# Kernel optimization log

Hardware: AMD Instinct MI355X
Metric: run time of the kernel (lower is better)

The kernel has to match this reference:

```python
import jax, jax.numpy as jnp
import numpy as np

SCALE = 768.0  # scale = output_features


def setup_inputs() -> dict:
    key = jax.random.key(0)
    k1, k2, k3, k4 = jax.random.split(key, 4)
    B, S, D, F = 8, 2048, 768, 768
    x = jax.random.normal(k1, (B, S, D), dtype=jnp.float32)
    # torch nn.Linear weights: shape (out_features, in_features), y = x @ W.T
    Wq = jax.random.normal(k2, (F, D), dtype=jnp.float32) * (1.0 / np.sqrt(D))
    Wk = jax.random.normal(k3, (F, D), dtype=jnp.float32) * (1.0 / np.sqrt(D))
    Wv = jax.random.normal(k4, (F, D), dtype=jnp.float32) * (1.0 / np.sqrt(D))
    return {"x": x, "Wq": Wq, "Wk": Wk, "Wv": Wv}


def _cdist_l2(q, k):
    # pairwise Euclidean distances, [B, S, S]; matches torch.cdist(q, k, p=2)
    q2 = jnp.sum(q * q, axis=-1)  # [B, S]
    k2 = jnp.sum(k * k, axis=-1)  # [B, S]
    qk = jnp.einsum('bid,bjd->bij', q, k)  # [B, S, S]
    d2 = q2[:, :, None] + k2[:, None, :] - 2.0 * qk
    return jnp.sqrt(jnp.maximum(d2, 0.0))


def reference(x, Wq, Wk, Wv):
    q = jnp.einsum('bsd,fd->bsf', x, Wq)
    k = jnp.einsum('bsd,fd->bsf', x, Wk)
    v = jnp.einsum('bsd,fd->bsf', x, Wv)
    scores = _cdist_l2(q, k) / jnp.sqrt(jnp.asarray(SCALE, dtype=x.dtype))
    attn = jax.nn.softmax(scores, axis=-1)  # NOTE: source softmaxes raw distances (no negation)
    return jnp.einsum('bij,bjf->bif', attn, v)
```

## Files before the change

kernel.cpp:

```cpp
#include <hip/hip_runtime.h>
#include <stdint.h>
#include <math.h>


typedef __attribute__((ext_vector_type(8))) __bf16 bf16x8;
typedef __attribute__((ext_vector_type(4))) float f32x4;
typedef __attribute__((ext_vector_type(4))) unsigned int u32x4;

__device__ __forceinline__ unsigned short f2b(float f) {
    unsigned u = __float_as_uint(f);
    unsigned r = 0x7fffu + ((u >> 16) & 1u);
    return (unsigned short)((u + r) >> 16);
}
__device__ __forceinline__ float b2f(unsigned short h) {
    return __uint_as_float(((unsigned)h) << 16);
}

__device__ __forceinline__ void wg_barrier() {
    asm volatile("" ::: "memory");
    __builtin_amdgcn_s_barrier();
    asm volatile("" ::: "memory");
}

__device__ __forceinline__ unsigned lds_off(const void* p) {
    return (unsigned)(uintptr_t)(const __attribute__((address_space(3))) char*)p;
}

__global__ __launch_bounds__(256) void castk(const float* __restrict__ src,
                                             unsigned short* __restrict__ dst, int n4) {
    int i = blockIdx.x * 256 + threadIdx.x;
    if (i >= n4) return;
    float4 v = ((const float4*)src)[i];
    ushort4 o;
    o.x = f2b(v.x); o.y = f2b(v.y); o.z = f2b(v.z); o.w = f2b(v.w);
    ((ushort4*)dst)[i] = o;
}

template <int MODE>
__global__ __launch_bounds__(256) void rowreduce(const unsigned short* __restrict__ X,
                                                 int L, int rows, float* __restrict__ out) {
    int w = threadIdx.x >> 6, lane = threadIdx.x & 63;
    int row = blockIdx.x * 4 + w;
    if (row >= rows) return;
    const unsigned short* xr = X + (size_t)row * L;
    float s = 0.f;
    int passes = L >> 8;
    for (int p = 0; p < passes; ++p) {
        ushort4 u = *(const ushort4*)(xr + (p << 8) + lane * 4);
        float a = b2f(u.x), b = b2f(u.y), c = b2f(u.z), d = b2f(u.w);
        s += MODE ? (a * a + b * b + c * c + d * d) : (a + b + c + d);
    }
#pragma unroll
    for (int o = 32; o > 0; o >>= 1) s += __shfl_down(s, o);
    if (lane == 0) out[row] = s;
}

#define MF(A_, B_, C_) (C_) = __builtin_amdgcn_mfma_f32_16x16x32_bf16((A_), (B_), (C_), 0, 0, 0)
#define DSR(dst_, a_, imm_) \
    asm volatile("ds_read_b128 %0, %1 offset:" #imm_ : "=v"(dst_) : "v"(a_))
#define GL4(d_, p_) asm volatile("global_load_dwordx4 %0, %1, off" : "=v"(d_) : "v"(p_))
#define DSW(a_, imm_, d_) \
    asm volatile("ds_write_b128 %0, %1 offset:" #imm_ :: "v"(a_), "v"(d_) : "memory")
#define LGKM(n_) asm volatile("s_waitcnt lgkmcnt(" #n_ ")" ::: "memory")
#define VMC0 asm volatile("s_waitcnt vmcnt(0)" ::: "memory")
#define SB0 __builtin_amdgcn_sched_barrier(0)

#define LOADT(T_) do {                                                     \
    const size_t ko_ = (size_t)(T_) * 64;                                  \
    GL4(ra0, pa + ko_);             GL4(ra1, pa + lda64 + ko_);            \
    GL4(ra2, pa + 2 * lda64 + ko_); GL4(ra3, pa + 3 * lda64 + ko_);        \
    GL4(rb0, pb + ko_);             GL4(rb1, pb + ldb64 + ko_);            \
    GL4(rb2, pb + 2 * ldb64 + ko_); GL4(rb3, pb + 3 * ldb64 + ko_);        \
} while (0)
#define WRITET(WB_) do {                                                   \
    const unsigned wa_ = wA + (WB_), wb2_ = wB + (WB_);                    \
    DSW(wa_, 0, ra0);     DSW(wa_, 8192, ra1);                             \
    DSW(wa_, 16384, ra2); DSW(wa_, 24576, ra3);                            \
    DSW(wb2_, 0, rb0);     DSW(wb2_, 8192, rb1);                           \
    DSW(wb2_, 16384, rb2); DSW(wb2_, 24576, rb3);                          \
} while (0)

template <int EPI>
__global__ __launch_bounds__(512, 2) void gemm256(
    const unsigned short* __restrict__ A, int lda, long long sA,
    const unsigned short* __restrict__ B, int ldb, long long sB,
    void* __restrict__ Cv, int ldc, long long sC,
    int Kd, int perm,
    const float* __restrict__ aux1, int sAux1,
    const float* __restrict__ aux2, int sAux2,
    float invs) {
    __shared__ __attribute__((aligned(128))) unsigned short As[2 * 256 * 64];
    __shared__ __attribute__((aligned(128))) unsigned short Bs[2 * 256 * 64];

    const int z = perm ? blockIdx.x : blockIdx.z;
    const int jb = perm ? blockIdx.y : blockIdx.x;
    const int ib = perm ? blockIdx.z : blockIdx.y;
    const unsigned short* __restrict__ Ab = A + (size_t)z * sA;
    const unsigned short* __restrict__ Bb = B + (size_t)z * sB;
    const int i0 = ib * 256;
    const int j0 = jb * 256;
    const int tid = threadIdx.x;
    const int w = tid >> 6, lane = tid & 63;
    const int wr = w >> 2, wc = w & 3;
    const int c16 = lane & 15, kq = lane >> 4;

    const int lr0 = tid >> 3;
    const int clog0 = (tid & 7) ^ (lr0 & 7);
    const unsigned short* pa = Ab + (size_t)(i0 + lr0) * lda + clog0 * 8;
    const unsigned short* pb = Bb + (size_t)(j0 + lr0) * ldb + clog0 * 8;
    const size_t lda64 = (size_t)64 * lda, ldb64 = (size_t)64 * ldb;

    const unsigned wA = lds_off(As) + (unsigned)tid * 16;
    const unsigned wB = lds_off(Bs) + (unsigned)tid * 16;

    const int swc = (kq ^ (c16 & 7)) << 4;
    const unsigned adrA0 = lds_off(As) + (unsigned)(wr * 128 + c16) * 128 + swc;
    const unsigned adrA0x = adrA0 ^ 64u;
    const unsigned adrB0 = lds_off(Bs) + (unsigned)(wc * 64 + c16) * 128 + swc;
    const unsigned adrB0x = adrB0 ^ 64u;

    f32x4 acc[8][4];
    const f32x4 zero = {0.f, 0.f, 0.f, 0.f};
#pragma unroll
    for (int i = 0; i < 8; ++i)
#pragma unroll
        for (int j = 0; j < 4; ++j) acc[i][j] = zero;

    u32x4 ra0, ra1, ra2, ra3, rb0, rb1, rb2, rb3;
    bf16x8 aL[4][2], aH[4][2], bF[4][2];

    const int nt = Kd >> 6;

    LOADT(0);
    VMC0;
    WRITET(0u);
    LOADT(1);
    LGKM(0);
    wg_barrier();

    for (int t = 0; t < nt; ++t) {
        const unsigned rb_ = (t & 1) ? 32768u : 0u;
        const unsigned wb_ = (t & 1) ? 0u : 32768u;
        const unsigned aA = adrA0 + rb_, aAx = adrA0x + rb_;
        const unsigned aB = adrB0 + rb_, aBx = adrB0x + rb_;
        DSR(aL[0][0], aA, 0);    DSR(aL[0][1], aAx, 0);
        DSR(aL[1][0], aA, 2048); DSR(aL[1][1], aAx, 2048);
        DSR(aL[2][0], aA, 4096); DSR(aL[2][1], aAx, 4096);
        DSR(aL[3][0], aA, 6144); DSR(aL[3][1], aAx, 6144);
        DSR(bF[0][0], aB, 0);    DSR(bF[0][1], aBx, 0);
        DSR(bF[1][0], aB, 2048); DSR(bF[1][1], aBx, 2048);
        DSR(bF[2][0], aB, 4096); DSR(bF[2][1], aBx, 4096);
        DSR(bF[3][0], aB, 6144); DSR(bF[3][1], aBx, 6144);
        if (t + 1 < nt) {
            VMC0;
            WRITET(wb_);
            if (t + 2 < nt) LOADT(t + 2);
            LGKM(8);
        } else {
            LGKM(0);
        }
        SB0;
        __builtin_amdgcn_s_setprio(1);
#pragma unroll
        for (int kk = 0; kk < 2; ++kk)
#pragma unroll
            for (int mi = 0; mi < 4; ++mi)
#pragma unroll
                for (int ni = 0; ni < 4; ++ni)
                    MF(aL[mi][kk], bF[ni][kk], acc[mi][ni]);
        __builtin_amdgcn_s_setprio(0);
        DSR(aH[0][0], aA, 8192);  DSR(aH[0][1], aAx, 8192);
        DSR(aH[1][0], aA, 10240); DSR(aH[1][1], aAx, 10240);
        DSR(aH[2][0], aA, 12288); DSR(aH[2][1], aAx, 12288);
        DSR(aH[3][0], aA, 14336); DSR(aH[3][1], aAx, 14336);
        LGKM(0); SB0;
        __builtin_amdgcn_s_setprio(1);
#pragma unroll
        for (int kk = 0; kk < 2; ++kk)
#pragma unroll
            for (int mi = 0; mi < 4; ++mi)
#pragma unroll
                for (int ni = 0; ni < 4; ++ni)
                    MF(aH[mi][kk], bF[ni][kk], acc[4 + mi][ni]);
        __builtin_amdgcn_s_setprio(0);
        wg_barrier();
    }

    const int r4 = kq * 4;
    if constexpr (EPI == 0) {
        unsigned short* C = (unsigned short*)Cv + (size_t)z * sC;
#pragma unroll
        for (int mi = 0; mi < 8; ++mi)
#pragma unroll
            for (int ni = 0; ni < 4; ++ni) {
                const int row = i0 + wr * 128 + mi * 16 + r4;
                const int col = j0 + wc * 64 + ni * 16 + c16;
#pragma unroll
                for (int r = 0; r < 4; ++r)
                    C[(size_t)(row + r) * ldc + col] = f2b(acc[mi][ni][r]);
            }
    } else if constexpr (EPI == 1) {
        unsigned short* C = (unsigned short*)Cv + (size_t)z * sC;
        const float* q2b = aux1 + (size_t)z * sAux1;
        const float* k2b = aux2 + (size_t)z * sAux2;
#pragma unroll
        for (int mi = 0; mi < 8; ++mi)
#pragma unroll
            for (int ni = 0; ni < 4; ++ni) {
                const int row = i0 + wr * 128 + mi * 16 + r4;
                const int col = j0 + wc * 64 + ni * 16 + c16;
                const float k2v = k2b[col];
#pragma unroll
                for (int r = 0; r < 4; ++r) {
                    float d2 = q2b[row + r] + k2v - 2.0f * acc[mi][ni][r];
                    float e = __expf(sqrtf(fmaxf(d2, 0.f)) * invs);
                    C[(size_t)(row + r) * ldc + col] = f2b(e);
                }
            }
    } else {
        float* C = (float*)Cv + (size_t)z * sC;
        const float* lb = aux1 + (size_t)z * sAux1;
#pragma unroll
        for (int mi = 0; mi < 8; ++mi)
#pragma unroll
            for (int ni = 0; ni < 4; ++ni) {
                const int row = i0 + wr * 128 + mi * 16 + r4;
                const int col = j0 + wc * 64 + ni * 16 + c16;
#pragma unroll
                for (int r = 0; r < 4; ++r)
                    C[(size_t)(row + r) * ldc + col] = acc[mi][ni][r] / lb[row + r];
            }
    }
}

extern "C" void kernel_launch(void* const* d_in, const int* in_sizes, int n_in,
                              void* d_out, int out_size, void* d_ws, size_t ws_size,
                              hipStream_t stream) {
    const float* x = (const float*)d_in[0];
    const float* Wq = (const float*)d_in[1];
    const float* Wk = (const float*)d_in[2];
    const float* Wv = (const float*)d_in[3];
    const int Bz = 8, S = 2048, D = 768, F = 768;
    const int BS = Bz * S;

    const size_t szX = (size_t)BS * D * 2;
    const size_t szW = (size_t)F * D * 2;
    const size_t szE = (size_t)Bz * S * S * 2;

    char* p = (char*)d_ws;
    unsigned short* xb = (unsigned short*)p;  p += szX;
    unsigned short* Wqb = (unsigned short*)p; p += szW;
    unsigned short* Wkb = (unsigned short*)p; p += szW;
    unsigned short* Wvb = (unsigned short*)p; p += szW;
    unsigned short* Qm = (unsigned short*)p;  p += szX;
    unsigned short* Km = (unsigned short*)p;  p += szX;
    unsigned short* VT = (unsigned short*)p;  p += szX;
    unsigned short* E = (unsigned short*)p;   p += szE;
    float* q2 = (float*)p;   p += (size_t)BS * 4;
    float* k2 = (float*)p;   p += (size_t)BS * 4;
    float* lsum = (float*)p; p += (size_t)BS * 4;
    if ((size_t)(p - (char*)d_ws) > ws_size) return;

    const float invs = 1.0f / sqrtf(768.0f);

    castk<<<(BS * D / 4 + 255) / 256, 256, 0, stream>>>(x, xb, BS * D / 4);
    castk<<<(F * D / 4 + 255) / 256, 256, 0, stream>>>(Wq, Wqb, F * D / 4);
    castk<<<(F * D / 4 + 255) / 256, 256, 0, stream>>>(Wk, Wkb, F * D / 4);
    castk<<<(F * D / 4 + 255) / 256, 256, 0, stream>>>(Wv, Wvb, F * D / 4);

    gemm256<0><<<dim3(F / 256, BS / 256, 2), 512, 0, stream>>>(
        xb, D, 0,
        Wqb, D, (long long)F * D,
        Qm, F, (long long)BS * F,
        D, 0, nullptr, 0, nullptr, 0, 0.f);

    gemm256<0><<<dim3(BS / 256, F / 256, 1), 512, 0, stream>>>(
        Wvb, D, 0,
        xb, D, 0,
        VT, BS, 0,
        D, 0, nullptr, 0, nullptr, 0, 0.f);

    rowreduce<1><<<BS / 4, 256, 0, stream>>>(Qm, F, BS, q2);
    rowreduce<1><<<BS / 4, 256, 0, stream>>>(Km, F, BS, k2);

    gemm256<1><<<dim3(Bz, S / 256, S / 256), 512, 0, stream>>>(
        Qm, F, (long long)S * F,
        Km, F, (long long)S * F,
        E, S, (long long)S * S,
        F, 1, q2, S, k2, S, invs);

    rowreduce<0><<<BS / 4, 256, 0, stream>>>(E, S, BS, lsum);

    gemm256<2><<<dim3(Bz, F / 256, S / 256), 512, 0, stream>>>(
        E, S, (long long)S * S,
        VT, BS, (long long)S,
        d_out, F, (long long)S * F,
        S, 1, lsum, S, nullptr, 0, 0.f);
}
```

Measured before the change: 254.1 us.

## Store Q and K in FP8 and compute distance GEMM with FP8 MFMA

The Q/K projection now writes FP8 e4m3 outputs instead of bf16. A new FP8 GEMM kernel computes QK^T using fp8 MFMA with half-width LDS tiles and loads, and fuses the exp(dist) epilogue. Row norms are computed from the FP8 values so they stay consistent with the dot products. This halves Q/K memory traffic and uses the higher-throughput FP8 matrix path, at the cost of precision. Distance errors feed straight into the exponent, so correctness tolerance is at risk.

```diff
diff --git a/kernel.cpp b/kernel.cpp
--- a/kernel.cpp
+++ b/kernel.cpp
@@ -1,4 +1,5 @@
 #include <hip/hip_runtime.h>
+#include <hip/hip_fp8.h>
 #include <stdint.h>
 #include <math.h>
 
@@ -6,6 +7,7 @@
 typedef __attribute__((ext_vector_type(8))) __bf16 bf16x8;
 typedef __attribute__((ext_vector_type(4))) float f32x4;
 typedef __attribute__((ext_vector_type(4))) unsigned int u32x4;
+typedef __attribute__((ext_vector_type(2))) unsigned int u32x2;
 
 __device__ __forceinline__ unsigned short f2b(float f) {
     unsigned u = __float_as_uint(f);
@@ -14,6 +16,15 @@
 }
 __device__ __forceinline__ float b2f(unsigned short h) {
     return __uint_as_float(((unsigned)h) << 16);
+}
+__device__ __forceinline__ unsigned char f2f8(float f) {
+    __hip_fp8_e4m3 t(f);
+    return t.__x;
+}
+__device__ __forceinline__ float f8tof(unsigned char b) {
+    int e = (b >> 3) & 15, m = b & 7;
+    float v = e ? ldexpf(8.0f + m, e - 10) : ldexpf((float)m, -9);
+    return (b & 0x80) ? -v : v;
 }
 
 __device__ __forceinline__ void wg_barrier() {
@@ -55,12 +66,36 @@
     if (lane == 0) out[row] = s;
 }
 
+__global__ __launch_bounds__(256) void rowreduce8(const unsigned char* __restrict__ X,
+                                                  int L, int rows, float* __restrict__ out) {
+    int w = threadIdx.x >> 6, lane = threadIdx.x & 63;
+    int row = blockIdx.x * 4 + w;
+    if (row >= rows) return;
+    const unsigned char* xr = X + (size_t)row * L;
+    float s = 0.f;
+    int passes = L >> 8;
+    for (int p = 0; p < passes; ++p) {
+        uchar4 u = *(const uchar4*)(xr + (p << 8) + lane * 4);
+        float a = f8tof(u.x), b = f8tof(u.y), c = f8tof(u.z), d = f8tof(u.w);
+        s += a * a + b * b + c * c + d * d;
+    }
+#pragma unroll
+    for (int o = 32; o > 0; o >>= 1) s += __shfl_down(s, o);
+    if (lane == 0) out[row] = s;
+}
+
 #define MF(A_, B_, C_) (C_) = __builtin_amdgcn_mfma_f32_16x16x32_bf16((A_), (B_), (C_), 0, 0, 0)
+#define MF8(A_, B_, C_) (C_) = __builtin_amdgcn_mfma_f32_16x16x32_fp8_fp8((A_), (B_), (C_), 0, 0, 0)
 #define DSR(dst_, a_, imm_) \
     asm volatile("ds_read_b128 %0, %1 offset:" #imm_ : "=v"(dst_) : "v"(a_))
+#define DSR64(dst_, a_, imm_) \
+    asm volatile("ds_read_b64 %0, %1 offset:" #imm_ : "=v"(dst_) : "v"(a_))
 #define GL4(d_, p_) asm volatile("global_load_dwordx4 %0, %1, off" : "=v"(d_) : "v"(p_))
+#define GL2(d_, p_) asm volatile("global_load_dwordx2 %0, %1, off" : "=v"(d_) : "v"(p_))
 #define DSW(a_, imm_, d_) \
     asm volatile("ds_write_b128 %0, %1 offset:" #imm_ :: "v"(a_), "v"(d_) : "memory")
+#define DSW64(a_, imm_, d_) \
+    asm volatile("ds_write_b64 %0, %1 offset:" #imm_ :: "v"(a_), "v"(d_) : "memory")
 #define LGKM(n_) asm volatile("s_waitcnt lgkmcnt(" #n_ ")" ::: "memory")
 #define VMC0 asm volatile("s_waitcnt vmcnt(0)" ::: "memory")
 #define SB0 __builtin_amdgcn_sched_barrier(0)
@@ -86,9 +121,7 @@
     const unsigned short* __restrict__ B, int ldb, long long sB,
     void* __restrict__ Cv, int ldc, long long sC,
     int Kd, int perm,
-    const float* __restrict__ aux1, int sAux1,
-    const float* __restrict__ aux2, int sAux2,
-    float invs) {
+    const float* __restrict__ aux1, int sAux1) {
     __shared__ __attribute__((aligned(128))) unsigned short As[2 * 256 * 64];
     __shared__ __attribute__((aligned(128))) unsigned short Bs[2 * 256 * 64];
 
@@ -97,8 +130,7 @@
     const int ib = perm ? blockIdx.z : blockIdx.y;
     const unsigned short* __restrict__ Ab = A + (size_t)z * sA;
     const unsigned short* __restrict__ Bb = B + (size_t)z * sB;
-    const int i0 = ib * 256;
-    const int j0 = jb * 256;
+    const int i0 = ib * 256, j0 = jb * 256;
     const int tid = threadIdx.x;
     const int w = tid >> 6, lane = tid & 63;
     const int wr = w >> 2, wc = w & 3;
@@ -199,23 +231,17 @@
                 for (int r = 0; r < 4; ++r)
                     C[(size_t)(row + r) * ldc + col] = f2b(acc[mi][ni][r]);
             }
-    } else if constexpr (EPI == 1) {
-        unsigned short* C = (unsigned short*)Cv + (size_t)z * sC;
-        const float* q2b = aux1 + (size_t)z * sAux1;
-        const float* k2b = aux2 + (size_t)z * sAux2;
+    } else if constexpr (EPI == 3) {
+        unsigned char* C = (unsigned char*)Cv + (size_t)z * sC;
 #pragma unroll
         for (int mi = 0; mi < 8; ++mi)
 #pragma unroll
             for (int ni = 0; ni < 4; ++ni) {
                 const int row = i0 + wr * 128 + mi * 16 + r4;
                 const int col = j0 + wc * 64 + ni * 16 + c16;
-                const float k2v = k2b[col];
-#pragma unroll
-                for (int r = 0; r < 4; ++r) {
-                    float d2 = q2b[row + r] + k2v - 2.0f * acc[mi][ni][r];
-                    float e = __expf(sqrtf(fmaxf(d2, 0.f)) * invs);
-                    C[(size_t)(row + r) * ldc + col] = f2b(e);
-                }
+#pragma unroll
+                for (int r = 0; r < 4; ++r)
+                    C[(size_t)(row + r) * ldc + col] = f2f8(acc[mi][ni][r]);
             }
     } else {
         float* C = (float*)Cv + (size_t)z * sC;
@@ -231,6 +257,144 @@
                     C[(size_t)(row + r) * ldc + col] = acc[mi][ni][r] / lb[row + r];
             }
     }
+}
+
+#define LOADT8(T_) do {                                                    \
+    const size_t ko_ = (size_t)(T_) * 64;                                  \
+    GL2(fa0, pa8 + ko_);              GL2(fa1, pa8 + lda64b + ko_);        \
+    GL2(fa2, pa8 + 2 * lda64b + ko_); GL2(fa3, pa8 + 3 * lda64b + ko_);    \
+    GL2(fb0, pb8 + ko_);              GL2(fb1, pb8 + ldb64b + ko_);        \
+    GL2(fb2, pb8 + 2 * ldb64b + ko_); GL2(fb3, pb8 + 3 * ldb64b + ko_);    \
+} while (0)
+#define WRITET8(WB_) do {                                                  \
+    const unsigned wa_ = wA8 + (WB_), wb2_ = wB8 + (WB_);                  \
+    DSW64(wa_, 0, fa0);     DSW64(wa_, 4096, fa1);                         \
+    DSW64(wa_, 8192, fa2);  DSW64(wa_, 12288, fa3);                        \
+    DSW64(wb2_, 0, fb0);    DSW64(wb2_, 4096, fb1);                        \
+    DSW64(wb2_, 8192, fb2); DSW64(wb2_, 12288, fb3);                       \
+} while (0)
+
+__global__ __launch_bounds__(512, 2) void gemm256f8(
+    const unsigned char* __restrict__ A, int lda, long long sA,
+    const unsigned char* __restrict__ B, int ldb, long long sB,
+    unsigned short* __restrict__ Cq, int ldc, long long sC,
+    int Kd,
+    const float* __restrict__ q2a, int sQ2,
+    const float* __restrict__ k2a, int sK2,
+    float invs) {
+    __shared__ __attribute__((aligned(128))) unsigned char As8[2 * 256 * 64];
+    __shared__ __attribute__((aligned(128))) unsigned char Bs8[2 * 256 * 64];
+
+    const int z = blockIdx.x;
+    const int jb = blockIdx.y, ib = blockIdx.z;
+    const unsigned char* __restrict__ Ab = A + (size_t)z * sA;
+    const unsigned char* __restrict__ Bb = B + (size_t)z * sB;
+    const int i0 = ib * 256, j0 = jb * 256;
+    const int tid = threadIdx.x;
+    const int w = tid >> 6, lane = tid & 63;
+    const int wr = w >> 2, wc = w & 3;
+    const int c16 = lane & 15, kq = lane >> 4;
+
+    const int lr0 = tid >> 3;
+    const int slog = (tid & 7) ^ (lr0 & 7);
+    const unsigned char* pa8 = Ab + (size_t)(i0 + lr0) * lda + slog * 8;
+    const unsigned char* pb8 = Bb + (size_t)(j0 + lr0) * ldb + slog * 8;
+    const size_t lda64b = (size_t)64 * lda, ldb64b = (size_t)64 * ldb;
+
+    const unsigned wA8 = lds_off(As8) + (unsigned)tid * 8;
+    const unsigned wB8 = lds_off(Bs8) + (unsigned)tid * 8;
+
+    const int sw8 = (kq ^ (c16 & 7)) << 3;
+    const unsigned adrA0 = lds_off(As8) + (unsigned)(wr * 128 + c16) * 64 + sw8;
+    const unsigned adrA0x = adrA0 ^ 32u;
+    const unsigned adrB0 = lds_off(Bs8) + (unsigned)(wc * 64 + c16) * 64 + sw8;
+    const unsigned adrB0x = adrB0 ^ 32u;
+
+    f32x4 acc[8][4];
+    const f32x4 zero = {0.f, 0.f, 0.f, 0.f};
+#pragma unroll
+    for (int i = 0; i < 8; ++i)
+#pragma unroll
+        for (int j = 0; j < 4; ++j) acc[i][j] = zero;
+
+    u32x2 fa0, fa1, fa2, fa3, fb0, fb1, fb2, fb3;
+    long aL[4][2], aH[4][2], bF[4][2];
+
+    const int nt = Kd >> 6;
+
+    LOADT8(0);
+    VMC0;
+    WRITET8(0u);
+    LOADT8(1);
+    LGKM(0);
+    wg_barrier();
+
+    for (int t = 0; t < nt; ++t) {
+        const unsigned rb_ = (t & 1) ? 16384u : 0u;
+        const unsigned wb_ = (t & 1) ? 0u : 16384u;
+        const unsigned aA = adrA0 + rb_, aAx = adrA0x + rb_;
+        const unsigned aB = adrB0 + rb_, aBx = adrB0x + rb_;
+        DSR64(aL[0][0], aA, 0);    DSR64(aL[0][1], aAx, 0);
+        DSR64(aL[1][0], aA, 1024); DSR64(aL[1][1], aAx, 1024);
+        DSR64(aL[2][0], aA, 2048); DSR64(aL[2][1], aAx, 2048);
+        DSR64(aL[3][0], aA, 3072); DSR64(aL[3][1], aAx, 3072);
+        DSR64(bF[0][0], aB, 0);    DSR64(bF[0][1], aBx, 0);
+        DSR64(bF[1][0], aB, 1024); DSR64(bF[1][1], aBx, 1024);
+        DSR64(bF[2][0], aB, 2048); DSR64(bF[2][1], aBx, 2048);
+        DSR64(bF[3][0], aB, 3072); DSR64(bF[3][1], aBx, 3072);
+        if (t + 1 < nt) {
+            VMC0;
+            WRITET8(wb_);
+            if (t + 2 < nt) LOADT8(t + 2);
+            LGKM(8);
+        } else {
+            LGKM(0);
+        }
+        SB0;
+        __builtin_amdgcn_s_setprio(1);
+#pragma unroll
+        for (int kk = 0; kk < 2; ++kk)
+#pragma unroll
+            for (int mi = 0; mi < 4; ++mi)
+#pragma unroll
+                for (int ni = 0; ni < 4; ++ni)
+                    MF8(aL[mi][kk], bF[ni][kk], acc[mi][ni]);
+        __builtin_amdgcn_s_setprio(0);
+        DSR64(aH[0][0], aA, 4096); DSR64(aH[0][1], aAx, 4096);
+        DSR64(aH[1][0], aA, 5120); DSR64(aH[1][1], aAx, 5120);
+        DSR64(aH[2][0], aA, 6144); DSR64(aH[2][1], aAx, 6144);
+        DSR64(aH[3][0], aA, 7168); DSR64(aH[3][1], aAx, 7168);
+        LGKM(0); SB0;
+        __builtin_amdgcn_s_setprio(1);
+#pragma unroll
+        for (int kk = 0; kk < 2; ++kk)
+#pragma unroll
+            for (int mi = 0; mi < 4; ++mi)
+#pragma unroll
+                for (int ni = 0; ni < 4; ++ni)
+                    MF8(aH[mi][kk], bF[ni][kk], acc[4 + mi][ni]);
+        __builtin_amdgcn_s_setprio(0);
+        wg_barrier();
+    }
+
+    const int r4 = kq * 4;
+    unsigned short* C = Cq + (size_t)z * sC;
+    const float* q2b = q2a + (size_t)z * sQ2;
+    const float* k2b = k2a + (size_t)z * sK2;
+#pragma unroll
+    for (int mi = 0; mi < 8; ++mi)
+#pragma unroll
+        for (int ni = 0; ni < 4; ++ni) {
+            const int row = i0 + wr * 128 + mi * 16 + r4;
+            const int col = j0 + wc * 64 + ni * 16 + c16;
+            const float k2v = k2b[col];
+#pragma unroll
+            for (int r = 0; r < 4; ++r) {
+                float d2 = q2b[row + r] + k2v - 2.0f * acc[mi][ni][r];
+                float e = __expf(sqrtf(fmaxf(d2, 0.f)) * invs);
+                C[(size_t)(row + r) * ldc + col] = f2b(e);
+            }
+        }
 }
 
 extern "C" void kernel_launch(void* const* d_in, const int* in_sizes, int n_in,
@@ -245,6 +409,7 @@
 
     const size_t szX = (size_t)BS * D * 2;
     const size_t szW = (size_t)F * D * 2;
+    const size_t szQ8 = (size_t)BS * F;
     const size_t szE = (size_t)Bz * S * S * 2;
 
     char* p = (char*)d_ws;
@@ -252,8 +417,8 @@
     unsigned short* Wqb = (unsigned short*)p; p += szW;
     unsigned short* Wkb = (unsigned short*)p; p += szW;
     unsigned short* Wvb = (unsigned short*)p; p += szW;
-    unsigned short* Qm = (unsigned short*)p;  p += szX;
-    unsigned short* Km = (unsigned short*)p;  p += szX;
+    unsigned char* Q8 = (unsigned char*)p;    p += szQ8;
+    unsigned char* K8 = (unsigned char*)p;    p += szQ8;
     unsigned short* VT = (unsigned short*)p;  p += szX;
     unsigned short* E = (unsigned short*)p;   p += szE;
     float* q2 = (float*)p;   p += (size_t)BS * 4;
@@ -268,26 +433,26 @@
     castk<<<(F * D / 4 + 255) / 256, 256, 0, stream>>>(Wk, Wkb, F * D / 4);
     castk<<<(F * D / 4 + 255) / 256, 256, 0, stream>>>(Wv, Wvb, F * D / 4);
 
-    gemm256<0><<<dim3(F / 256, BS / 256, 2), 512, 0, stream>>>(
+    gemm256<3><<<dim3(F / 256, BS / 256, 2), 512, 0, stream>>>(
         xb, D, 0,
         Wqb, D, (long long)F * D,
-        Qm, F, (long long)BS * F,
-        D, 0, nullptr, 0, nullptr, 0, 0.f);
+        Q8, F, (long long)BS * F,
+        D, 0, nullptr, 0);
 
     gemm256<0><<<dim3(BS / 256, F / 256, 1), 512, 0, stream>>>(
         Wvb, D, 0,
         xb, D, 0,
         VT, BS, 0,
-        D, 0, nullptr, 0, nullptr, 0, 0.f);
-
-    rowreduce<1><<<BS / 4, 256, 0, stream>>>(Qm, F, BS, q2);
-    rowreduce<1><<<BS / 4, 256, 0, stream>>>(Km, F, BS, k2);
-
-    gemm256<1><<<dim3(Bz, S / 256, S / 256), 512, 0, stream>>>(
-        Qm, F, (long long)S * F,
-        Km, F, (long long)S * F,
+        D, 0, nullptr, 0);
+
+    rowreduce8<<<BS / 4, 256, 0, stream>>>(Q8, F, BS, q2);
+    rowreduce8<<<BS / 4, 256, 0, stream>>>(K8, F, BS, k2);
+
+    gemm256f8<<<dim3(Bz, S / 256, S / 256), 512, 0, stream>>>(
+        Q8, F, (long long)S * F,
+        K8, F, (long long)S * F,
         E, S, (long long)S * S,
-        F, 1, q2, S, k2, S, invs);
+        F, q2, S, k2, S, invs);
 
     rowreduce<0><<<BS / 4, 256, 0, stream>>>(E, S, BS, lsum);
 
@@ -295,5 +460,5 @@
         E, S, (long long)S * S,
         VT, BS, (long long)S,
         d_out, F, (long long)S * F,
-        S, 1, lsum, S, nullptr, 0, 0.f);
-}
+        S, 1, lsum, S);
+}
```

Result: faster. 246.0 us (-3.2%).
